# Performance work log

Hardware: AMD Instinct MI355X
Metric: run time of the kernel (lower is better)

Reference implementation:

```python
import jax, jax.numpy as jnp
import numpy as np

FSIZE = 5
PAD = FSIZE // 2


def _conv(mosaick, filts):
    # mosaick [B,1,H,W], filts [f,f,K] -> responses [B,K,H,W].
    # Cross-correlation with edge-clamped boundary (Halide clamp semantics).
    x = jnp.pad(mosaick, ((0, 0), (0, 0), (PAD, PAD), (PAD, PAD)), mode='edge')
    k = jnp.transpose(filts, (2, 0, 1))[:, None, :, :]  # [K,1,f,f] OIHW
    return jax.lax.conv_general_dilated(
        x, k, window_strides=(1, 1), padding='VALID',
        dimension_numbers=('NCHW', 'OIHW', 'NCHW'))


def setup_inputs() -> dict:
    key = jax.random.key(0)
    k1, k2, k3 = jax.random.split(key, 3)
    B, H, W, K, f = 16, 512, 512, 8, FSIZE
    std = 1.0 / (f * f)  # matches normal_(0, 1/(fsize*fsize))
    return {
        'mosaick': jax.random.normal(k1, (B, 1, H, W), dtype=jnp.float32),
        'sel_filts': jax.random.normal(k2, (f, f, K), dtype=jnp.float32) * std,
        'green_filts': jax.random.normal(k3, (f, f, K), dtype=jnp.float32) * std,
    }


def reference(mosaick, sel_filts, green_filts):
    # Per-pixel soft filter selection over K candidate green-interpolation filters.
    sel = _conv(mosaick, sel_filts)      # [B,K,H,W] selection scores
    grn = _conv(mosaick, green_filts)    # [B,K,H,W] candidate green estimates
    w = jax.nn.softmax(sel, axis=1)      # softmax over filter bank
    interp = jnp.sum(w * grn, axis=1, keepdims=True)  # [B,1,H,W]
    # GRBG Bayer: green where row parity == col parity; copy known greens.
    H, W = mosaick.shape[-2], mosaick.shape[-1]
    yy = jnp.arange(H)[:, None]
    xx = jnp.arange(W)[None, :]
    is_green = (yy % 2) == (xx % 2)      # [H,W] bool
    # Output green channel only (module returns output[:, 1:2, ...]).
    return jnp.where(is_green, mosaick, interp)
```

## Files before the change

### kernel.cpp

```cpp
#include <hip/hip_runtime.h>


typedef float f32x16 __attribute__((ext_vector_type(16)));
typedef short s16x8  __attribute__((ext_vector_type(8)));

#define HH 512
#define WW 512
#define TW 64
#define TH 16
#define RS 80
#define NROW 20
#define NEL 72

__device__ __forceinline__ unsigned short bf16rne(float x) {
    unsigned u = __float_as_uint(x);
    u += 0x7fffu + ((u >> 16) & 1u);
    return (unsigned short)(u >> 16);
}
__device__ __forceinline__ int pk2(float hi, float lo) {
    return (int)((((unsigned)bf16rne(hi)) << 16) | (unsigned)bf16rne(lo));
}
__device__ __forceinline__ float hi16(int v) { return __uint_as_float(((unsigned)v) & 0xffff0000u); }
__device__ __forceinline__ float lo16(int v) { return __uint_as_float(((unsigned)v) << 16); }

__global__ void build_frags_kernel(const float* __restrict__ sf,
                                   const float* __restrict__ gf,
                                   short* __restrict__ ws)
{
    const int lane = threadIdx.x;
    const int mm   = lane & 31;
    const int h    = (lane >> 5) & 1;
    const int c    = mm >> 1;
    const bool tg  = mm & 1;
    const bool chok = mm < 16;
    const float* fb = tg ? gf : sf;

    s16x8 A[6];
#pragma unroll
    for (int f = 0; f < 6; ++f)
#pragma unroll
        for (int j = 0; j < 8; ++j) A[f][j] = 0;

#pragma unroll
    for (int j = 0; j < 8; ++j) {
        const int dx0 = j - 1;
        if (dx0 >= 0 && dx0 < 5 && chok) {
            A[0][j] = (short)bf16rne(fb[((h)     * 5 + dx0) * 8 + c]);
            A[1][j] = (short)bf16rne(fb[((2 + h) * 5 + dx0) * 8 + c]);
            if (h == 0)
                A[2][j] = (short)bf16rne(fb[(4 * 5 + dx0) * 8 + c]);
        }
        const int dx1 = j;
        if (dx1 < 5 && chok) {
            if (h == 1)
                A[3][j] = (short)bf16rne(fb[(0 * 5 + dx1) * 8 + c]);
            A[4][j] = (short)bf16rne(fb[((1 + h) * 5 + dx1) * 8 + c]);
            A[5][j] = (short)bf16rne(fb[((3 + h) * 5 + dx1) * 8 + c]);
        }
    }
    s16x8* dst = (s16x8*)(ws + lane * 48);
#pragma unroll
    for (int f = 0; f < 6; ++f) dst[f] = A[f];
}

__global__ __launch_bounds__(256) void demosaick_kernel(
    const float* __restrict__ mos,
    const short* __restrict__ frg,
    float* __restrict__ out)
{
    __shared__ alignas(16) unsigned short tileS[NROW * RS];

    const int tid   = threadIdx.x;
    const int bx    = blockIdx.x;
    const int by    = blockIdx.y;
    const int bimg  = blockIdx.z;
    const int tileX = bx * TW;
    const int tileY = by * TH;
    const float* img = mos + (size_t)bimg * HH * WW;

    const int lane = tid & 63;
    const int w    = tid >> 6;
    const int n    = lane & 31;
    const int h    = lane >> 5;

    const s16x8* wsf = (const s16x8*)(frg + lane * 48);
    const s16x8 Aa0 = wsf[0], Ab0 = wsf[1], Ac0 = wsf[2];
    const s16x8 Aa1 = wsf[3], Ab1 = wsf[4], Ac1 = wsf[5];

    const bool interior = (bx >= 1) && (bx <= 6) && (by >= 1) && (by <= 30);
    if (interior) {
        if (tid < 180) {
            int r = tid / 9, s = tid - 9 * r;
            const float2* src = (const float2*)(img + (size_t)(tileY - 2 + r) * WW
                                                + (tileX - 2 + 8 * s));
            float2 v0 = src[0], v1 = src[1], v2 = src[2], v3 = src[3];
            int4 d;
            d.x = pk2(v0.y, v0.x);
            d.y = pk2(v1.y, v1.x);
            d.z = pk2(v2.y, v2.x);
            d.w = pk2(v3.y, v3.x);
            *(int4*)&tileS[r * RS + 8 * s] = d;
        }
    } else {
        for (int i = tid; i < NROW * NEL; i += 256) {
            int r = i / NEL, e = i - NEL * r;
            int gy = min(max(tileY - 2 + r, 0), HH - 1);
            int gx = min(max(tileX - 2 + e, 0), WW - 1);
            tileS[r * RS + e] = bf16rne(img[(size_t)gy * WW + gx]);
        }
    }
    __syncthreads();

    const int* tb = (const int*)tileS;

    union { int4 v; s16x8 s; } B[4];
#pragma unroll
    for (int r = 0; r < 4; ++r) {
        const int ia = (4 * w + 2 * r + h) * 40 + n;
        B[r].v.x = tb[ia];     B[r].v.y = tb[ia + 1];
        B[r].v.z = tb[ia + 2]; B[r].v.w = tb[ia + 3];
    }

    f32x16 a00 = (f32x16)(0.f), a01 = (f32x16)(0.f);
    f32x16 a10 = (f32x16)(0.f), a11 = (f32x16)(0.f);
    a00 = __builtin_amdgcn_mfma_f32_32x32x16_bf16(Aa0, B[0].s, a00, 0, 0, 0);
    a01 = __builtin_amdgcn_mfma_f32_32x32x16_bf16(Aa1, B[0].s, a01, 0, 0, 0);
    a10 = __builtin_amdgcn_mfma_f32_32x32x16_bf16(Aa0, B[1].s, a10, 0, 0, 0);
    a11 = __builtin_amdgcn_mfma_f32_32x32x16_bf16(Aa1, B[1].s, a11, 0, 0, 0);
    a00 = __builtin_amdgcn_mfma_f32_32x32x16_bf16(Ab0, B[1].s, a00, 0, 0, 0);
    a01 = __builtin_amdgcn_mfma_f32_32x32x16_bf16(Ab1, B[1].s, a01, 0, 0, 0);
    a10 = __builtin_amdgcn_mfma_f32_32x32x16_bf16(Ab0, B[2].s, a10, 0, 0, 0);
    a11 = __builtin_amdgcn_mfma_f32_32x32x16_bf16(Ab1, B[2].s, a11, 0, 0, 0);
    a00 = __builtin_amdgcn_mfma_f32_32x32x16_bf16(Ac0, B[2].s, a00, 0, 0, 0);
    a01 = __builtin_amdgcn_mfma_f32_32x32x16_bf16(Ac1, B[2].s, a01, 0, 0, 0);
    a10 = __builtin_amdgcn_mfma_f32_32x32x16_bf16(Ac0, B[3].s, a10, 0, 0, 0);
    a11 = __builtin_amdgcn_mfma_f32_32x32x16_bf16(Ac1, B[3].s, a11, 0, 0, 0);

    float nums[4], dens[4];
    {
        const f32x16* av[4] = { &a00, &a01, &a10, &a11 };
#pragma unroll
        for (int r = 0; r < 4; ++r) {
            float den = 0.f, num = 0.f;
            const f32x16& a = *av[r];
#pragma unroll
            for (int j = 0; j < 4; ++j) {
                float e = __expf(a[2 * j]);
                den += e;
                num = fmaf(e, a[2 * j + 1], num);
            }
            nums[r] = num; dens[r] = den;
        }
    }

    const int nd0 = pk2(nums[0], dens[0]);
    const int nd1 = pk2(nums[1], dens[1]);
    const int nd2 = pk2(nums[2], dens[2]);
    const int nd3 = pk2(nums[3], dens[3]);

    const int send0 = h ? nd0 : nd2;
    const int send1 = h ? nd1 : nd3;
    const int rec0  = __shfl_xor(send0, 32);
    const int rec1  = __shfl_xor(send1, 32);
    const int mine0 = h ? nd2 : nd0;
    const int mine1 = h ? nd3 : nd1;

    const float numA = hi16(mine0) + hi16(rec0);
    const float denA = lo16(mine0) + lo16(rec0);
    const float numB = hi16(mine1) + hi16(rec1);
    const float denB = lo16(mine1) + lo16(rec1);
    const float interpA = numA * __builtin_amdgcn_rcpf(denA);
    const float interpB = numB * __builtin_amdgcn_rcpf(denB);

    float* outp = out + (size_t)bimg * HH * WW;
    const int y  = tileY + 4 * w + 2 * h;
    const int x0 = tileX + 2 * n;

    const float greenA = img[(size_t)y * WW + x0];
    const float greenB = img[(size_t)(y + 1) * WW + x0 + 1];
    float2 stA; stA.x = greenA;  stA.y = interpA;
    float2 stB; stB.x = interpB; stB.y = greenB;
    *(float2*)(outp + (size_t)y * WW + x0)       = stA;
    *(float2*)(outp + (size_t)(y + 1) * WW + x0) = stB;
}

extern "C" void kernel_launch(void* const* d_in, const int* in_sizes, int n_in,
                              void* d_out, int out_size, void* d_ws, size_t ws_size,
                              hipStream_t stream) {
    const float* mos = (const float*)d_in[0];
    const float* sf  = (const float*)d_in[1];
    const float* gf  = (const float*)d_in[2];
    float* out = (float*)d_out;
    short* ws  = (short*)d_ws;

    const int B = in_sizes[0] / (HH * WW);

    build_frags_kernel<<<1, 64, 0, stream>>>(sf, gf, ws);

    dim3 grid(WW / TW, HH / TH, B);
    dim3 block(256);
    demosaick_kernel<<<grid, block, 0, stream>>>(mos, (const short*)ws, out);
}
```

Measured before the change: 86.77 us.

## Double tile height and slide B fragments across row pairs per wave

Doubles the tile height, so each block stages 36 halo rows instead of 20 and the relative halo overhead shrinks. Each wave now walks 4 row pairs, keeping a sliding window of three B fragments in registers and reloading only one per step. The exact green copy is now read from the bf16 LDS tile instead of global fp32 memory, which removes a global read but rounds those pixels to bf16 precision. Stores come only from the half-wave with h==0, and the grid has half as many blocks, which reduces parallelism.

```diff
diff --git a/kernel.cpp b/kernel.cpp
--- a/kernel.cpp
+++ b/kernel.cpp
@@ -7,9 +7,9 @@
 #define HH 512
 #define WW 512
 #define TW 64
-#define TH 16
+#define TH 32
 #define RS 80
-#define NROW 20
+#define NROW 36
 #define NEL 72
 
 __device__ __forceinline__ unsigned short bf16rne(float x) {
@@ -22,6 +22,9 @@
 }
 __device__ __forceinline__ float hi16(int v) { return __uint_as_float(((unsigned)v) & 0xffff0000u); }
 __device__ __forceinline__ float lo16(int v) { return __uint_as_float(((unsigned)v) << 16); }
+__device__ __forceinline__ float bf2f(unsigned short s) {
+    return __uint_as_float(((unsigned)s) << 16);
+}
 
 __global__ void build_frags_kernel(const float* __restrict__ sf,
                                    const float* __restrict__ gf,
@@ -87,10 +90,10 @@
     const s16x8 Aa0 = wsf[0], Ab0 = wsf[1], Ac0 = wsf[2];
     const s16x8 Aa1 = wsf[3], Ab1 = wsf[4], Ac1 = wsf[5];
 
-    const bool interior = (bx >= 1) && (bx <= 6) && (by >= 1) && (by <= 30);
+    const bool interior = (bx >= 1) && (bx <= 6) && (by >= 1) && (by <= 14);
     if (interior) {
-        if (tid < 180) {
-            int r = tid / 9, s = tid - 9 * r;
+        for (int i = tid; i < NROW * 9; i += 256) {
+            int r = i / 9, s = i - 9 * r;
             const float2* src = (const float2*)(img + (size_t)(tileY - 2 + r) * WW
                                                 + (tileX - 2 + 8 * s));
             float2 v0 = src[0], v1 = src[1], v2 = src[2], v3 = src[3];
@@ -112,76 +115,71 @@
     __syncthreads();
 
     const int* tb = (const int*)tileS;
-
-    union { int4 v; s16x8 s; } B[4];
-#pragma unroll
-    for (int r = 0; r < 4; ++r) {
-        const int ia = (4 * w + 2 * r + h) * 40 + n;
-        B[r].v.x = tb[ia];     B[r].v.y = tb[ia + 1];
-        B[r].v.z = tb[ia + 2]; B[r].v.w = tb[ia + 3];
-    }
-
-    f32x16 a00 = (f32x16)(0.f), a01 = (f32x16)(0.f);
-    f32x16 a10 = (f32x16)(0.f), a11 = (f32x16)(0.f);
-    a00 = __builtin_amdgcn_mfma_f32_32x32x16_bf16(Aa0, B[0].s, a00, 0, 0, 0);
-    a01 = __builtin_amdgcn_mfma_f32_32x32x16_bf16(Aa1, B[0].s, a01, 0, 0, 0);
-    a10 = __builtin_amdgcn_mfma_f32_32x32x16_bf16(Aa0, B[1].s, a10, 0, 0, 0);
-    a11 = __builtin_amdgcn_mfma_f32_32x32x16_bf16(Aa1, B[1].s, a11, 0, 0, 0);
-    a00 = __builtin_amdgcn_mfma_f32_32x32x16_bf16(Ab0, B[1].s, a00, 0, 0, 0);
-    a01 = __builtin_amdgcn_mfma_f32_32x32x16_bf16(Ab1, B[1].s, a01, 0, 0, 0);
-    a10 = __builtin_amdgcn_mfma_f32_32x32x16_bf16(Ab0, B[2].s, a10, 0, 0, 0);
-    a11 = __builtin_amdgcn_mfma_f32_32x32x16_bf16(Ab1, B[2].s, a11, 0, 0, 0);
-    a00 = __builtin_amdgcn_mfma_f32_32x32x16_bf16(Ac0, B[2].s, a00, 0, 0, 0);
-    a01 = __builtin_amdgcn_mfma_f32_32x32x16_bf16(Ac1, B[2].s, a01, 0, 0, 0);
-    a10 = __builtin_amdgcn_mfma_f32_32x32x16_bf16(Ac0, B[3].s, a10, 0, 0, 0);
-    a11 = __builtin_amdgcn_mfma_f32_32x32x16_bf16(Ac1, B[3].s, a11, 0, 0, 0);
-
-    float nums[4], dens[4];
+    float* outp = out + (size_t)bimg * HH * WW;
+
+    union U { int4 v; s16x8 s; };
+    U B0, B1, B2;
     {
-        const f32x16* av[4] = { &a00, &a01, &a10, &a11 };
-#pragma unroll
-        for (int r = 0; r < 4; ++r) {
-            float den = 0.f, num = 0.f;
-            const f32x16& a = *av[r];
-#pragma unroll
-            for (int j = 0; j < 4; ++j) {
-                float e = __expf(a[2 * j]);
-                den += e;
-                num = fmaf(e, a[2 * j + 1], num);
-            }
-            nums[r] = num; dens[r] = den;
-        }
-    }
-
-    const int nd0 = pk2(nums[0], dens[0]);
-    const int nd1 = pk2(nums[1], dens[1]);
-    const int nd2 = pk2(nums[2], dens[2]);
-    const int nd3 = pk2(nums[3], dens[3]);
-
-    const int send0 = h ? nd0 : nd2;
-    const int send1 = h ? nd1 : nd3;
-    const int rec0  = __shfl_xor(send0, 32);
-    const int rec1  = __shfl_xor(send1, 32);
-    const int mine0 = h ? nd2 : nd0;
-    const int mine1 = h ? nd3 : nd1;
-
-    const float numA = hi16(mine0) + hi16(rec0);
-    const float denA = lo16(mine0) + lo16(rec0);
-    const float numB = hi16(mine1) + hi16(rec1);
-    const float denB = lo16(mine1) + lo16(rec1);
-    const float interpA = numA * __builtin_amdgcn_rcpf(denA);
-    const float interpB = numB * __builtin_amdgcn_rcpf(denB);
-
-    float* outp = out + (size_t)bimg * HH * WW;
-    const int y  = tileY + 4 * w + 2 * h;
-    const int x0 = tileX + 2 * n;
-
-    const float greenA = img[(size_t)y * WW + x0];
-    const float greenB = img[(size_t)(y + 1) * WW + x0 + 1];
-    float2 stA; stA.x = greenA;  stA.y = interpA;
-    float2 stB; stB.x = interpB; stB.y = greenB;
-    *(float2*)(outp + (size_t)y * WW + x0)       = stA;
-    *(float2*)(outp + (size_t)(y + 1) * WW + x0) = stB;
+        const int ia0 = (8 * w + h) * 40 + n;
+        B0.v.x = tb[ia0];       B0.v.y = tb[ia0 + 1];
+        B0.v.z = tb[ia0 + 2];   B0.v.w = tb[ia0 + 3];
+        B1.v.x = tb[ia0 + 80];  B1.v.y = tb[ia0 + 81];
+        B1.v.z = tb[ia0 + 82];  B1.v.w = tb[ia0 + 83];
+        B2.v.x = tb[ia0 + 160]; B2.v.y = tb[ia0 + 161];
+        B2.v.z = tb[ia0 + 162]; B2.v.w = tb[ia0 + 163];
+    }
+
+#pragma unroll
+    for (int pp = 0; pp < 4; ++pp) {
+        const int Rl = 8 * w + 2 * pp;
+        const int y  = tileY + Rl;
+
+        f32x16 a0 = (f32x16)(0.f), a1 = (f32x16)(0.f);
+        a0 = __builtin_amdgcn_mfma_f32_32x32x16_bf16(Aa0, B0.s, a0, 0, 0, 0);
+        a1 = __builtin_amdgcn_mfma_f32_32x32x16_bf16(Aa1, B0.s, a1, 0, 0, 0);
+        a0 = __builtin_amdgcn_mfma_f32_32x32x16_bf16(Ab0, B1.s, a0, 0, 0, 0);
+        a1 = __builtin_amdgcn_mfma_f32_32x32x16_bf16(Ab1, B1.s, a1, 0, 0, 0);
+        a0 = __builtin_amdgcn_mfma_f32_32x32x16_bf16(Ac0, B2.s, a0, 0, 0, 0);
+        a1 = __builtin_amdgcn_mfma_f32_32x32x16_bf16(Ac1, B2.s, a1, 0, 0, 0);
+
+        if (pp < 3) {
+            B0 = B1; B1 = B2;
+            const int ia = (Rl + 6 + h) * 40 + n;
+            B2.v.x = tb[ia];     B2.v.y = tb[ia + 1];
+            B2.v.z = tb[ia + 2]; B2.v.w = tb[ia + 3];
+        }
+
+        float den0 = 0.f, num0 = 0.f, den1 = 0.f, num1 = 0.f;
+#pragma unroll
+        for (int j = 0; j < 4; ++j) {
+            float e0 = __expf(a0[2 * j]);
+            den0 += e0;
+            num0 = fmaf(e0, a0[2 * j + 1], num0);
+            float e1 = __expf(a1[2 * j]);
+            den1 += e1;
+            num1 = fmaf(e1, a1[2 * j + 1], num1);
+        }
+        int ndA  = pk2(num0, den0);
+        int ndB  = pk2(num1, den1);
+        int ndA2 = __shfl_xor(ndA, 32);
+        int ndB2 = __shfl_xor(ndB, 32);
+        const float numA = num0 + hi16(ndA2);
+        const float denA = den0 + lo16(ndA2);
+        const float numB = num1 + hi16(ndB2);
+        const float denB = den1 + lo16(ndB2);
+        const float interpA = numA * __builtin_amdgcn_rcpf(denA);
+        const float interpB = numB * __builtin_amdgcn_rcpf(denB);
+
+        if (h == 0) {
+            const int x0 = tileX + 2 * n;
+            const float greenA = bf2f(tileS[(Rl + 2) * RS + 2 * n + 2]);
+            const float greenB = bf2f(tileS[(Rl + 3) * RS + 2 * n + 3]);
+            float2 stA; stA.x = greenA;  stA.y = interpA;
+            float2 stB; stB.x = interpB; stB.y = greenB;
+            *(float2*)(outp + (size_t)y * WW + x0)       = stA;
+            *(float2*)(outp + (size_t)(y + 1) * WW + x0) = stB;
+        }
+    }
 }
 
 extern "C" void kernel_launch(void* const* d_in, const int* in_sizes, int n_in,
```

New measurement: 86.04 us. About the same (-0.8%).
